# Kernel optimization log

Measured on AMD Instinct MI355X. Metric: run time of the kernel, lower is better.

Reference implementation:

```python
import jax, jax.numpy as jnp
import numpy as np

NUM_HEADS = 16


def _apply_rope(x, freqs):
    # x: (H, L, C), freqs: (L, C//2); computed in fp32, cast back to x.dtype
    xf = x.astype(jnp.float32)
    x1, x2 = jnp.split(xf, 2, axis=-1)
    f = freqs.astype(jnp.float32)[None]  # (1, L, C//2)
    cos, sin = jnp.cos(f), jnp.sin(f)
    out = jnp.concatenate((x1 * cos - x2 * sin, x1 * sin + x2 * cos), axis=-1)
    return out.astype(x.dtype)


def setup_inputs() -> dict:
    key = jax.random.key(0)
    k0, k1, k2, k3 = jax.random.split(key, 4)
    S, D, H = 4096, 1280, NUM_HEADS
    hd = D // H
    hidden_states = jax.random.normal(k0, (S, D), dtype=jnp.float32)
    cu_seqlens = jnp.array([0, 1024, 2048, 3072, 4096], dtype=jnp.int32)
    rotary_pos_emb = jax.random.normal(k1, (S, hd // 2), dtype=jnp.float32)
    scale = 1.0 / np.sqrt(D)
    w_qkv = (jax.random.normal(k2, (D, 3 * D), dtype=jnp.float32) * scale)
    b_qkv = jnp.zeros((3 * D,), dtype=jnp.float32)
    w_proj = (jax.random.normal(k3, (D, D), dtype=jnp.float32) * scale)
    b_proj = jnp.zeros((D,), dtype=jnp.float32)
    return {
        "hidden_states": hidden_states,
        "cu_seqlens": cu_seqlens,
        "rotary_pos_emb": rotary_pos_emb,
        "w_qkv": w_qkv,
        "b_qkv": b_qkv,
        "w_proj": w_proj,
        "b_proj": b_proj,
    }


def reference(hidden_states, cu_seqlens, rotary_pos_emb, w_qkv, b_qkv, w_proj, b_proj):
    S, D = hidden_states.shape
    H = NUM_HEADS
    hd = D // H
    qkv = hidden_states @ w_qkv + b_qkv            # (S, 3D)
    qkv = qkv.reshape(S, 3, H, hd).transpose(1, 2, 0, 3)  # (3, H, S, hd)
    q, k, v = qkv[0], qkv[1], qkv[2]
    q = _apply_rope(q, rotary_pos_emb)
    k = _apply_rope(k, rotary_pos_emb)
    # block-diagonal (per-segment) attention, equivalent to the per-segment loop
    seg = jnp.searchsorted(cu_seqlens, jnp.arange(S), side="right") - 1  # (S,)
    mask = seg[:, None] == seg[None, :]            # (S, S)
    scores = jnp.einsum("hqd,hkd->hqk", q, k) / np.sqrt(hd)
    scores = jnp.where(mask[None], scores, -jnp.inf)
    attn = jax.nn.softmax(scores.astype(jnp.float32), axis=-1).astype(q.dtype)
    out = jnp.einsum("hqk,hkd->qhd", attn, v).reshape(S, D)
    return out @ w_proj + b_proj
```

## Files before the change

kernel.cpp:

```cpp
#include <hip/hip_runtime.h>
#include <hip/hip_bf16.h>
#include <cstdint>

typedef __bf16 bf16x8 __attribute__((ext_vector_type(8)));
typedef __bf16 bf16x4 __attribute__((ext_vector_type(4)));
typedef short short4_ __attribute__((ext_vector_type(4)));
typedef float f32x4 __attribute__((ext_vector_type(4)));

#define SLEN 4096
#define DMODEL 1280
#define NHEADS 16
#define HD 80
#define HDP 96
#define KROW 104
#define VTILE_ELEMS 3328
#define VTILE_LDS 3584

#define GLD_LDS16(g, l)                                                        \
  __builtin_amdgcn_global_load_lds(                                            \
      (const __attribute__((address_space(1))) void*)(g),                      \
      (__attribute__((address_space(3))) void*)(l), 16, 0, 0)

#define WAIT_VMCNT(n) __builtin_amdgcn_s_waitcnt((n & 0xF) | 0x70 | 0xF00 | ((n >> 4) << 14))

__global__ __launch_bounds__(256) void cvt_f32_bf16(const float* __restrict__ in,
                                                    __bf16* __restrict__ out, int n4) {
  int i = blockIdx.x * 256 + threadIdx.x;
  if (i < n4) {
    float4 v = ((const float4*)in)[i];
    bf16x4 o = { (__bf16)v.x, (__bf16)v.y, (__bf16)v.z, (__bf16)v.w };
    ((bf16x4*)out)[i] = o;
  }
}

__global__ __launch_bounds__(256) void transpose_cvt(const float* __restrict__ in,
                                                     __bf16* __restrict__ out,
                                                     int K, int N) {
  __shared__ float tile[32][33];
  int n0 = blockIdx.x * 32, k0 = blockIdx.y * 32;
  int x = threadIdx.x & 31, y = threadIdx.x >> 5;
  for (int i = 0; i < 32; i += 8)
    tile[y + i][x] = in[(size_t)(k0 + y + i) * N + n0 + x];
  __syncthreads();
  for (int i = 0; i < 32; i += 8)
    out[(size_t)(n0 + y + i) * K + k0 + x] = (__bf16)tile[x][y + i];
}

template <int WMW>
__global__ __launch_bounds__(WMW * 2 * 64) void gemm_bt(const __bf16* __restrict__ A,
                                                        const __bf16* __restrict__ Bt,
                                                        const float* __restrict__ bias,
                                                        void* __restrict__ C,
                                                        int M, int N, int K, int store_bf16) {
  constexpr int BM = WMW * 64;
  constexpr int NW = WMW * 2;
  constexpr int BI = 8 / NW;
  constexpr int PW = 2 + BI;
  constexpr int ASZ = BM * 32, BSZ = 128 * 32;

  __shared__ __attribute__((aligned(16))) __bf16 As[3][ASZ];
  __shared__ __attribute__((aligned(16))) __bf16 Bs[3][BSZ];

  const int t = threadIdx.x;
  const int lane = t & 63, wave = t >> 6;
  const int quad = lane >> 4, l15 = lane & 15;
  const int wm = (wave & (WMW - 1)) * 64, wn = (wave / WMW) * 64;
  const int bm = blockIdx.x * BM, bn = blockIdx.y * 128;

  const int rs = lane >> 2, cs = (lane & 3) * 8;
  const __bf16* AgQ[2];
  const __bf16* BgQ[BI];
  int aLds[2], bLds[BI];
#pragma unroll
  for (int q = 0; q < 2; ++q) {
    int row = (wave * 2 + q) * 16;
    AgQ[q] = A + (size_t)(bm + row + rs) * K + cs;
    aLds[q] = row * 32;
  }
#pragma unroll
  for (int q = 0; q < BI; ++q) {
    int row = (wave * BI + q) * 16;
    BgQ[q] = Bt + (size_t)(bn + row + rs) * K + cs;
    bLds[q] = row * 32;
  }

  f32x4 acc[4][4] = {};
  const int niter = K >> 5;

#pragma unroll
  for (int s = 0; s < 2; ++s) {
#pragma unroll
    for (int q = 0; q < 2; ++q) GLD_LDS16(AgQ[q] + s * 32, &As[s][aLds[q]]);
#pragma unroll
    for (int q = 0; q < BI; ++q) GLD_LDS16(BgQ[q] + s * 32, &Bs[s][bLds[q]]);
  }

  int cmp = 0, stg = 2;
  for (int it = 0; it < niter; ++it) {
    const int kk = (it + 2 < niter ? it + 2 : niter - 1) * 32;
#pragma unroll
    for (int q = 0; q < 2; ++q) GLD_LDS16(AgQ[q] + kk, &As[stg][aLds[q]]);
#pragma unroll
    for (int q = 0; q < BI; ++q) GLD_LDS16(BgQ[q] + kk, &Bs[stg][bLds[q]]);
    asm volatile("" ::: "memory");
    WAIT_VMCNT(2 * PW);
    __builtin_amdgcn_s_barrier();
    asm volatile("" ::: "memory");

    bf16x8 af[4], bfr[4];
#pragma unroll
    for (int i = 0; i < 4; ++i)
      af[i] = *(const bf16x8*)&As[cmp][(wm + i * 16 + l15) * 32 + quad * 8];
#pragma unroll
    for (int j = 0; j < 4; ++j)
      bfr[j] = *(const bf16x8*)&Bs[cmp][(wn + j * 16 + l15) * 32 + quad * 8];
#pragma unroll
    for (int i = 0; i < 4; ++i)
#pragma unroll
      for (int j = 0; j < 4; ++j)
        acc[i][j] = __builtin_amdgcn_mfma_f32_16x16x32_bf16(af[i], bfr[j], acc[i][j], 0, 0, 0);

    asm volatile("" ::: "memory");
    __builtin_amdgcn_s_barrier();
    asm volatile("" ::: "memory");
    cmp = (cmp == 2) ? 0 : cmp + 1;
    stg = (stg == 2) ? 0 : stg + 1;
  }

  for (int j = 0; j < 4; ++j) {
    int col = bn + wn + j * 16 + l15;
    float bv = bias[col];
    for (int i = 0; i < 4; ++i) {
      int r0 = bm + wm + i * 16 + quad * 4;
      for (int r = 0; r < 4; ++r) {
        float v = acc[i][j][r] + bv;
        if (store_bf16)
          ((__bf16*)C)[(size_t)(r0 + r) * N + col] = (__bf16)v;
        else
          ((float*)C)[(size_t)(r0 + r) * N + col] = v;
      }
    }
  }
}

__global__ __launch_bounds__(256) void rope_pack(const __bf16* __restrict__ qkv,
                                                 const float* __restrict__ freqs,
                                                 __bf16* __restrict__ qp,
                                                 __bf16* __restrict__ kp,
                                                 __bf16* __restrict__ vt) {
  const float QSCALE = 0.11180339887498949f * 1.44269504088896340f;
  int h = blockIdx.y;
  int s0 = blockIdx.x * 64;
  int t = threadIdx.x;
  int sp = t >> 2, l4 = t & 3;
  int s = s0 + sp;
  const __bf16* row = qkv + (size_t)s * 3840 + h * 80;
  __bf16* qo = qp + (size_t)(h * SLEN + s) * HDP;
  __bf16* ko = kp + (size_t)(h * SLEN + s) * KROW;

#pragma unroll
  for (int k = 0; k < 10; ++k) {
    int j = l4 * 10 + k;
    float f = freqs[s * 40 + j];
    float cs = __builtin_cosf(f), sn = __builtin_sinf(f);
    float x1 = (float)row[j], x2 = (float)row[j + 40];
    float y1 = (float)row[1280 + j], y2 = (float)row[1280 + j + 40];
    qo[j]      = (__bf16)((x1 * cs - x2 * sn) * QSCALE);
    qo[j + 40] = (__bf16)((x1 * sn + x2 * cs) * QSCALE);
    ko[j]      = (__bf16)(y1 * cs - y2 * sn);
    ko[j + 40] = (__bf16)(y1 * sn + y2 * cs);
  }
#pragma unroll
  for (int k = 0; k < 4; ++k) {
    int c = 80 + l4 * 4 + k;
    qo[c] = (__bf16)0.f;
    ko[c] = (__bf16)0.f;
  }

  __shared__ float vtile[64][81];
#pragma unroll
  for (int k = 0; k < 20; ++k) {
    int d = l4 * 20 + k;
    vtile[sp][d] = (float)row[2560 + d];
  }
  __syncthreads();
  int key = t & 31, g8 = t >> 5;
  for (int c2 = 0; c2 < 2; ++c2) {
    __bf16* tb = vt + (size_t)(h * (SLEN / 32) + (s0 >> 5) + c2) * VTILE_ELEMS;
#pragma unroll
    for (int k = 0; k < 10; ++k) {
      int d = g8 * 10 + k;
      tb[d * 40 + key] = (__bf16)vtile[c2 * 32 + key][d];
    }
  }
}

__global__ __launch_bounds__(256) void flash_attn(const __bf16* __restrict__ qp,
                                                  const __bf16* __restrict__ kp,
                                                  const __bf16* __restrict__ vt,
                                                  const int* __restrict__ cu, int nseg,
                                                  __bf16* __restrict__ out) {
  const float MEXP = 16.0f;
  int h = blockIdx.y;
  int q0 = blockIdx.x * 64;
  int seg = 0;
  for (int i = 1; i < nseg; ++i)
    if (cu[i] <= q0) seg = i;
  int kstart = cu[seg], kend = cu[seg + 1];

  int t = threadIdx.x;
  int lane = t & 63, wave = t >> 6;
  int quad = lane >> 4, l15 = lane & 15;

  __shared__ __attribute__((aligned(16))) __bf16 Ks[64 * KROW];
  __shared__ __attribute__((aligned(16))) __bf16 Vs[2 * VTILE_LDS];

  bf16x8 qf[3];
  {
    const __bf16* qptr = qp + (size_t)(h * SLEN + q0 + wave * 16 + l15) * HDP + quad * 8;
    qf[0] = *(const bf16x8*)(qptr);
    qf[1] = *(const bf16x8*)(qptr + 32);
    qf[2] = *(const bf16x8*)(qptr + 64);
  }

  f32x4 o[5] = {};
  float l_p = 0.f;

  const __bf16* gK = kp + (size_t)(h * SLEN + kstart) * KROW + lane * 8;
  const __bf16* gV = vt + (size_t)(h * (SLEN / 32) + (kstart >> 5)) * VTILE_ELEMS + lane * 8;

  int niter = (kend - kstart) >> 6;

  for (int it = 0; it < niter; ++it) {
    __syncthreads();
    for (int i = wave; i < 13; i += 4)
      GLD_LDS16(gK + i * 512, &Ks[i * 512]);
    for (int i = wave; i < 7; i += 4)
      GLD_LDS16(gV + i * 512, &Vs[i * 512]);
    for (int i = wave; i < 7; i += 4)
      GLD_LDS16(gV + VTILE_ELEMS + i * 512, &Vs[VTILE_LDS + i * 512]);
    gK += 64 * KROW;
    gV += 2 * VTILE_ELEMS;
    __syncthreads();

    f32x4 sc[4];
#pragma unroll
    for (int nt = 0; nt < 4; ++nt) {
      sc[nt] = f32x4{-MEXP, -MEXP, -MEXP, -MEXP};
#pragma unroll
      for (int c = 0; c < 3; ++c) {
        bf16x8 kf = *(const bf16x8*)&Ks[(nt * 16 + l15) * KROW + quad * 8 + c * 32];
        sc[nt] = __builtin_amdgcn_mfma_f32_16x16x32_bf16(kf, qf[c], sc[nt], 0, 0, 0);
      }
    }

    bf16x4 pf[4];
#pragma unroll
    for (int nt = 0; nt < 4; ++nt)
#pragma unroll
      for (int r = 0; r < 4; ++r) {
        float p = __builtin_amdgcn_exp2f(sc[nt][r]);
        l_p += p;
        pf[nt][r] = (__bf16)p;
      }

#pragma unroll
    for (int kq = 0; kq < 4; ++kq) {
      int vbase = (kq >> 1) * VTILE_LDS + (kq & 1) * 16 + quad * 4;
#pragma unroll
      for (int dt = 0; dt < 5; ++dt) {
        bf16x4 vfr = *(const bf16x4*)&Vs[vbase + (dt * 16 + l15) * 40];
        o[dt] = __builtin_amdgcn_mfma_f32_16x16x16bf16_1k(
            *(short4_*)&vfr, *(short4_*)&pf[kq], o[dt], 0, 0, 0);
      }
    }
  }

  l_p += __shfl_xor(l_p, 16);
  l_p += __shfl_xor(l_p, 32);
  float rinv = 1.0f / l_p;

  int qrow = q0 + wave * 16 + l15;
#pragma unroll
  for (int dt = 0; dt < 5; ++dt) {
    bf16x4 ov;
#pragma unroll
    for (int r = 0; r < 4; ++r)
      ov[r] = (__bf16)(o[dt][r] * rinv);
    *(bf16x4*)&out[(size_t)qrow * DMODEL + h * 80 + dt * 16 + quad * 4] = ov;
  }
}

extern "C" void kernel_launch(void* const* d_in, const int* in_sizes, int n_in,
                              void* d_out, int out_size, void* d_ws, size_t ws_size,
                              hipStream_t stream) {
  const float* hidden = (const float*)d_in[0];
  const int* cu       = (const int*)d_in[1];
  const float* freqs  = (const float*)d_in[2];
  const float* w_qkv  = (const float*)d_in[3];
  const float* b_qkv  = (const float*)d_in[4];
  const float* w_proj = (const float*)d_in[5];
  const float* b_proj = (const float*)d_in[6];
  float* out = (float*)d_out;

  char* ws = (char*)d_ws;
  size_t off = 0;
  auto alloc = [&](size_t bytes) {
    char* p = ws + off;
    off += (bytes + 255) & ~(size_t)255;
    return p;
  };
  __bf16* hid_b  = (__bf16*)alloc((size_t)SLEN * DMODEL * 2);
  __bf16* wqkvT  = (__bf16*)alloc((size_t)3840 * 1280 * 2);
  __bf16* wprojT = (__bf16*)alloc((size_t)1280 * 1280 * 2);
  __bf16* qkvb   = (__bf16*)alloc((size_t)SLEN * 3840 * 2);
  __bf16* qp     = (__bf16*)alloc((size_t)NHEADS * SLEN * HDP * 2);
  __bf16* kp     = (__bf16*)alloc((size_t)NHEADS * SLEN * KROW * 2 + 1024);
  __bf16* vt     = (__bf16*)alloc((size_t)NHEADS * (SLEN / 32) * VTILE_ELEMS * 2 + 1024);
  __bf16* attn   = hid_b;

  cvt_f32_bf16<<<(SLEN * DMODEL / 4 + 255) / 256, 256, 0, stream>>>(hidden, hid_b, SLEN * DMODEL / 4);
  transpose_cvt<<<dim3(3840 / 32, 1280 / 32), 256, 0, stream>>>(w_qkv, wqkvT, 1280, 3840);
  transpose_cvt<<<dim3(1280 / 32, 1280 / 32), 256, 0, stream>>>(w_proj, wprojT, 1280, 1280);
  gemm_bt<4><<<dim3(SLEN / 256, 3840 / 128), 512, 0, stream>>>(hid_b, wqkvT, b_qkv, qkvb,
                                                               SLEN, 3840, 1280, 1);
  rope_pack<<<dim3(SLEN / 64, NHEADS), 256, 0, stream>>>(qkvb, freqs, qp, kp, vt);
  int nseg = in_sizes[1] - 1;
  flash_attn<<<dim3(SLEN / 64, NHEADS), 256, 0, stream>>>(qp, kp, vt, cu, nseg, attn);
  gemm_bt<2><<<dim3(SLEN / 128, DMODEL / 128), 256, 0, stream>>>(attn, wprojT, b_proj, out,
                                                                 SLEN, DMODEL, 1280, 0);
}
```

Measured before the change: 251.7 us.

## Double-buffer K/V tiles and use 128-query blocks in flash attention

The attention kernel now uses 8 waves covering 128 queries per block, so each K/V tile loaded into LDS is shared by twice as many queries. K/V loads go into two LDS buffers: the next tile is prefetched with async global-to-LDS loads while the current one is computed, synchronised by a vmcnt wait plus barriers. This is meant to hide global load latency and halve K/V traffic per query. The costs are more LDS per block, fewer blocks in flight, and a redundant reload of the last tile on the final iteration.

After: 247.6 us. Within noise of the previous version (-1.6%).

```diff
diff --git a/kernel.cpp b/kernel.cpp
--- a/kernel.cpp
+++ b/kernel.cpp
@@ -195,14 +195,14 @@
   }
 }
 
-__global__ __launch_bounds__(256) void flash_attn(const __bf16* __restrict__ qp,
+__global__ __launch_bounds__(512) void flash_attn(const __bf16* __restrict__ qp,
                                                   const __bf16* __restrict__ kp,
                                                   const __bf16* __restrict__ vt,
                                                   const int* __restrict__ cu, int nseg,
                                                   __bf16* __restrict__ out) {
   const float MEXP = 16.0f;
   int h = blockIdx.y;
-  int q0 = blockIdx.x * 64;
+  int q0 = blockIdx.x * 128;
   int seg = 0;
   for (int i = 1; i < nseg; ++i)
     if (cu[i] <= q0) seg = i;
@@ -212,8 +212,8 @@
   int lane = t & 63, wave = t >> 6;
   int quad = lane >> 4, l15 = lane & 15;
 
-  __shared__ __attribute__((aligned(16))) __bf16 Ks[64 * KROW];
-  __shared__ __attribute__((aligned(16))) __bf16 Vs[2 * VTILE_LDS];
+  __shared__ __attribute__((aligned(16))) __bf16 Ks[2][64 * KROW];
+  __shared__ __attribute__((aligned(16))) __bf16 Vs[2][2 * VTILE_LDS];
 
   bf16x8 qf[3];
   {
@@ -229,19 +229,34 @@
   const __bf16* gK = kp + (size_t)(h * SLEN + kstart) * KROW + lane * 8;
   const __bf16* gV = vt + (size_t)(h * (SLEN / 32) + (kstart >> 5)) * VTILE_ELEMS + lane * 8;
 
-  int niter = (kend - kstart) >> 6;
+  const int niter = (kend - kstart) >> 6;
+
+  auto stage = [&](int kn, int buf) {
+#pragma unroll
+    for (int i0 = 0; i0 < 4; ++i0) {
+      int i = wave + i0 * 8;
+      int ii = i < 27 ? i : 26;
+      if (ii < 13)
+        GLD_LDS16(gK + (size_t)kn * (64 * KROW) + ii * 512, &Ks[buf][ii * 512]);
+      else if (ii < 20)
+        GLD_LDS16(gV + (size_t)kn * (2 * VTILE_ELEMS) + (ii - 13) * 512,
+                  &Vs[buf][(ii - 13) * 512]);
+      else
+        GLD_LDS16(gV + (size_t)kn * (2 * VTILE_ELEMS) + VTILE_ELEMS + (ii - 20) * 512,
+                  &Vs[buf][VTILE_LDS + (ii - 20) * 512]);
+    }
+  };
+
+  stage(0, 0);
 
   for (int it = 0; it < niter; ++it) {
-    __syncthreads();
-    for (int i = wave; i < 13; i += 4)
-      GLD_LDS16(gK + i * 512, &Ks[i * 512]);
-    for (int i = wave; i < 7; i += 4)
-      GLD_LDS16(gV + i * 512, &Vs[i * 512]);
-    for (int i = wave; i < 7; i += 4)
-      GLD_LDS16(gV + VTILE_ELEMS + i * 512, &Vs[VTILE_LDS + i * 512]);
-    gK += 64 * KROW;
-    gV += 2 * VTILE_ELEMS;
-    __syncthreads();
+    const int cur = it & 1, nxt = cur ^ 1;
+    const int kn = (it + 1 < niter) ? it + 1 : niter - 1;
+    stage(kn, nxt);
+    asm volatile("" ::: "memory");
+    WAIT_VMCNT(4);
+    __builtin_amdgcn_s_barrier();
+    asm volatile("" ::: "memory");
 
     f32x4 sc[4];
 #pragma unroll
@@ -249,7 +264,7 @@
       sc[nt] = f32x4{-MEXP, -MEXP, -MEXP, -MEXP};
 #pragma unroll
       for (int c = 0; c < 3; ++c) {
-        bf16x8 kf = *(const bf16x8*)&Ks[(nt * 16 + l15) * KROW + quad * 8 + c * 32];
+        bf16x8 kf = *(const bf16x8*)&Ks[cur][(nt * 16 + l15) * KROW + quad * 8 + c * 32];
         sc[nt] = __builtin_amdgcn_mfma_f32_16x16x32_bf16(kf, qf[c], sc[nt], 0, 0, 0);
       }
     }
@@ -269,11 +284,15 @@
       int vbase = (kq >> 1) * VTILE_LDS + (kq & 1) * 16 + quad * 4;
 #pragma unroll
       for (int dt = 0; dt < 5; ++dt) {
-        bf16x4 vfr = *(const bf16x4*)&Vs[vbase + (dt * 16 + l15) * 40];
+        bf16x4 vfr = *(const bf16x4*)&Vs[cur][vbase + (dt * 16 + l15) * 40];
         o[dt] = __builtin_amdgcn_mfma_f32_16x16x16bf16_1k(
             *(short4_*)&vfr, *(short4_*)&pf[kq], o[dt], 0, 0, 0);
       }
     }
+
+    asm volatile("" ::: "memory");
+    __builtin_amdgcn_s_barrier();
+    asm volatile("" ::: "memory");
   }
 
   l_p += __shfl_xor(l_p, 16);
@@ -326,7 +345,7 @@
                                                                SLEN, 3840, 1280, 1);
   rope_pack<<<dim3(SLEN / 64, NHEADS), 256, 0, stream>>>(qkvb, freqs, qp, kp, vt);
   int nseg = in_sizes[1] - 1;
-  flash_attn<<<dim3(SLEN / 64, NHEADS), 256, 0, stream>>>(qp, kp, vt, cu, nseg, attn);
+  flash_attn<<<dim3(SLEN / 128, NHEADS), 512, 0, stream>>>(qp, kp, vt, cu, nseg, attn);
   gemm_bt<2><<<dim3(SLEN / 128, DMODEL / 128), 256, 0, stream>>>(attn, wprojT, b_proj, out,
                                                                  SLEN, DMODEL, 1280, 0);
 }
```
